# Kernel optimization log

Hardware: AMD Instinct MI355X
Metric: run time of the kernel (lower is better)

## Reference

```python
import jax, jax.numpy as jnp
import numpy as np

N = 100000
E = 1600000
IN_C = 128
OUT_C = 128


def setup_inputs() -> dict:
    key = jax.random.key(0)
    k1, k2, k3, k4, k5, k6 = jax.random.split(key, 6)
    x = jax.random.normal(k1, (N, IN_C), dtype=jnp.float32)
    edge_row = jax.random.randint(k2, (E,), 0, N, dtype=jnp.int32)  # dst nodes
    edge_col = jax.random.randint(k3, (E,), 0, N, dtype=jnp.int32)  # src nodes
    scale = 1.0 / np.sqrt(IN_C)
    W_l = jax.random.normal(k4, (IN_C, OUT_C), dtype=jnp.float32) * scale
    b_l = jax.random.normal(k5, (OUT_C,), dtype=jnp.float32) * 0.01
    W_r = jax.random.normal(k6, (IN_C, OUT_C), dtype=jnp.float32) * scale
    return {"x": x, "edge_row": edge_row, "edge_col": edge_col,
            "W_l": W_l, "b_l": b_l, "W_r": W_r}


def reference(x, edge_row, edge_col, W_l, b_l, W_r):
    # SAGEConv with mean aggregation over adj_t (edge_row=dst, edge_col=src)
    msgs = x[edge_col]                                   # [E, IN_C] gather
    summed = jax.ops.segment_sum(msgs, edge_row, num_segments=N)  # [N, IN_C]
    deg = jax.ops.segment_sum(jnp.ones((E,), dtype=x.dtype), edge_row,
                              num_segments=N)            # [N]
    agg = summed / jnp.maximum(deg, 1.0)[:, None]        # mean aggregation
    out = agg @ W_l + b_l + x @ W_r                      # lin_l(agg) + lin_r(x_dst)
    return jax.nn.relu(out)
```

## Files before the change

kernel.cpp:

```cpp
#include <hip/hip_runtime.h>

#define N_NODES 100000
#define E_EDGES 1600000
#define C 128
#define BSHIFT 10
#define NBKT 98
#define CAP 18432

typedef __attribute__((ext_vector_type(8))) short short8;
typedef __attribute__((ext_vector_type(4))) float f32x4;

__device__ __forceinline__ unsigned short f2bf(float f) {
  unsigned int b = __float_as_uint(f);
  return (unsigned short)((b + 0x7fffu + ((b >> 16) & 1u)) >> 16);
}
__device__ __forceinline__ float bflo(unsigned int v) {
  return __uint_as_float(v << 16);
}
__device__ __forceinline__ float bfhi(unsigned int v) {
  return __uint_as_float(v & 0xffff0000u);
}

__global__ __launch_bounds__(256) void cvt_kernel(const float* __restrict__ x,
                                                  ushort* __restrict__ xh) {
  int t = blockIdx.x * 256 + threadIdx.x;
  float4 a = ((const float4*)x)[2 * t];
  float4 b = ((const float4*)x)[2 * t + 1];
  ushort u[8] = {f2bf(a.x), f2bf(a.y), f2bf(a.z), f2bf(a.w),
                 f2bf(b.x), f2bf(b.y), f2bf(b.z), f2bf(b.w)};
  ((uint4*)xh)[t] = *(const uint4*)u;
}

__global__ __launch_bounds__(256) void pack_kernel(const float* __restrict__ W_l,
                                                   const float* __restrict__ W_r,
                                                   ushort* __restrict__ Bp) {
  int t = blockIdx.x * 256 + threadIdx.x;
  int Cb = t >> 9, kb = (t >> 6) & 7, lane = t & 63;
  int n = Cb * 16 + (lane & 15);
  int k0 = kb * 32 + (lane >> 4) * 8;
  ushort u[8];
#pragma unroll
  for (int j = 0; j < 8; ++j) {
    int k = k0 + j;
    float w = (k < C) ? W_l[k * C + n] : W_r[(k - C) * C + n];
    u[j] = f2bf(w);
  }
  ((uint4*)Bp)[t] = *(const uint4*)u;
}

__global__ __launch_bounds__(512) void passA_kernel(
    const int* __restrict__ erow, const int* __restrict__ ecol,
    int* __restrict__ bcnt, int* __restrict__ pairs) {
  __shared__ int cnt[NBKT], pos[NBKT], loff[NBKT], total;
  __shared__ int lbuf[2048];
  __shared__ int gaddr[2048];
  int tid = threadIdx.x;
  int idx = blockIdx.x * 512 + tid;
  for (int b = tid; b < NBKT; b += 512) cnt[b] = 0;
  __syncthreads();

  bool ok = (idx < E_EDGES / 4);
  int4 r, c;
  int bk[4], rk[4];
  if (ok) {
    r = ((const int4*)erow)[idx];
    c = ((const int4*)ecol)[idx];
    bk[0] = r.x >> BSHIFT; rk[0] = atomicAdd(&cnt[bk[0]], 1);
    bk[1] = r.y >> BSHIFT; rk[1] = atomicAdd(&cnt[bk[1]], 1);
    bk[2] = r.z >> BSHIFT; rk[2] = atomicAdd(&cnt[bk[2]], 1);
    bk[3] = r.w >> BSHIFT; rk[3] = atomicAdd(&cnt[bk[3]], 1);
  }
  __syncthreads();

  if (tid < NBKT) pos[tid] = atomicAdd(&bcnt[tid], cnt[tid]);
  if (tid == 0) {
    int run = 0;
    for (int b = 0; b < NBKT; ++b) { loff[b] = run; run += cnt[b]; }
    total = run;
  }
  __syncthreads();

  if (ok) {
    int src[4] = {c.x, c.y, c.z, c.w};
    int dst[4] = {r.x, r.y, r.z, r.w};
#pragma unroll
    for (int i = 0; i < 4; ++i) {
      int s = loff[bk[i]] + rk[i];
      lbuf[s] = (src[i] << BSHIFT) | (dst[i] & (  (1<<BSHIFT) - 1));
      int g = pos[bk[i]] + rk[i];
      gaddr[s] = (g < CAP) ? bk[i] * CAP + g : -1;
    }
  }
  __syncthreads();

  int tot = total;
  for (int i = tid; i < tot; i += 512) {
    int g = gaddr[i];
    if (g >= 0) pairs[g] = lbuf[i];
  }
}

__global__ __launch_bounds__(128) void bscan_kernel(const int* __restrict__ bcnt,
                                                    int* __restrict__ bbase) {
  __shared__ int l[128];
  int t = threadIdx.x;
  int v = (t < NBKT) ? min(bcnt[t], CAP) : 0;
  l[t] = v;
  __syncthreads();
  for (int d = 1; d < 128; d <<= 1) {
    int u = (t >= d) ? l[t - d] : 0;
    __syncthreads();
    l[t] += u;
    __syncthreads();
  }
  if (t < NBKT) bbase[t] = l[t] - v;
}

__global__ __launch_bounds__(1024) void passB_kernel(
    const int* __restrict__ pairs, const int* __restrict__ bcnt,
    const int* __restrict__ bbase, int* __restrict__ off,
    int* __restrict__ ssrc) {
  __shared__ int l[1024];
  __shared__ int cur[1024];
  int b = blockIdx.x, t = threadIdx.x;
  int nbase = b << BSHIFT;
  int nn = min(1024, N_NODES - nbase);
  int cnt = min(bcnt[b], CAP);
  int gbase = bbase[b];
  const int* bp = pairs + b * CAP;

  l[t] = 0;
  __syncthreads();
  for (int e = t; e < cnt; e += 1024) atomicAdd(&l[bp[e] & 1023], 1);
  __syncthreads();
  int own = l[t];
  for (int d = 1; d < 1024; d <<= 1) {
    int u = (t >= d) ? l[t - d] : 0;
    __syncthreads();
    l[t] += u;
    __syncthreads();
  }
  int excl = l[t] - own;
  if (t < nn) { off[nbase + t] = gbase + excl; cur[t] = excl; }
  if (b == NBKT - 1 && t == 1023) off[N_NODES] = gbase + l[1023];
  __syncthreads();
  for (int e = t; e < cnt; e += 1024) {
    int p = bp[e];
    int pos = atomicAdd(&cur[p & 1023], 1);
    ssrc[gbase + pos] = p >> BSHIFT;
  }
}

__global__ __launch_bounds__(256) void fused_kernel(
    const ushort* __restrict__ xh, const int* __restrict__ off,
    const int* __restrict__ ssrc, const ushort* __restrict__ Bp,
    const float* __restrict__ b_l, float* __restrict__ out) {
  __shared__ ushort lA[32][264];
  int tid = threadIdx.x;
  int lane = tid & 63;
  int wave = tid >> 6;
  long base = (long)blockIdx.x * 32;

  for (int i = tid; i < 32 * 16; i += 256) {
    int r = i >> 4, q = i & 15;
    uint4 v = ((const uint4*)(xh + (base + r) * C))[q];
    *(uint4*)&lA[r][128 + q * 8] = v;
  }

  int l4 = lane & 15;
  int q = lane >> 4;

  for (int j = 0; j < 8; ++j) {
    int n = wave * 8 + j;
    long row = base + n;
    int e0 = off[row];
    int e1 = off[row + 1];
    float s[8];
#pragma unroll
    for (int i = 0; i < 8; ++i) s[i] = 0.0f;

    int e = e0 + q;
    for (; e + 4 < e1; e += 8) {
      int sa = ssrc[e];
      int sb = ssrc[e + 4];
      uint4 va = ((const uint4*)(xh + (long)sa * C))[l4];
      uint4 vb = ((const uint4*)(xh + (long)sb * C))[l4];
      s[0] += bflo(va.x) + bflo(vb.x); s[1] += bfhi(va.x) + bfhi(vb.x);
      s[2] += bflo(va.y) + bflo(vb.y); s[3] += bfhi(va.y) + bfhi(vb.y);
      s[4] += bflo(va.z) + bflo(vb.z); s[5] += bfhi(va.z) + bfhi(vb.z);
      s[6] += bflo(va.w) + bflo(vb.w); s[7] += bfhi(va.w) + bfhi(vb.w);
    }
    if (e < e1) {
      int sa = ssrc[e];
      uint4 va = ((const uint4*)(xh + (long)sa * C))[l4];
      s[0] += bflo(va.x); s[1] += bfhi(va.x);
      s[2] += bflo(va.y); s[3] += bfhi(va.y);
      s[4] += bflo(va.z); s[5] += bfhi(va.z);
      s[6] += bflo(va.w); s[7] += bfhi(va.w);
    }
#pragma unroll
    for (int i = 0; i < 8; ++i) {
      s[i] += __shfl_xor(s[i], 16);
      s[i] += __shfl_xor(s[i], 32);
    }
    float inv = 1.0f / fmaxf((float)(e1 - e0), 1.0f);
    if (q == 0) {
      ushort u[8];
#pragma unroll
      for (int i = 0; i < 8; ++i) u[i] = f2bf(s[i] * inv);
      *(uint4*)&lA[n][l4 * 8] = *(const uint4*)u;
    }
  }
  __syncthreads();

  f32x4 acc0 = {0, 0, 0, 0}, acc1 = {0, 0, 0, 0};
  f32x4 acc2 = {0, 0, 0, 0}, acc3 = {0, 0, 0, 0};
  int m = lane & 15, quad = lane >> 4;
  const ushort* bp0 = Bp + (((2 * wave + 0) * 8) * 64 + lane) * 8;
  const ushort* bp1 = Bp + (((2 * wave + 1) * 8) * 64 + lane) * 8;
#pragma unroll
  for (int kb = 0; kb < 8; ++kb) {
    short8 a0 = *(const short8*)&lA[m][kb * 32 + quad * 8];
    short8 a1 = *(const short8*)&lA[16 + m][kb * 32 + quad * 8];
    short8 b0 = *(const short8*)(bp0 + kb * 64 * 8);
    short8 b1 = *(const short8*)(bp1 + kb * 64 * 8);
    acc0 = __builtin_amdgcn_mfma_f32_16x16x32_bf16(a0, b0, acc0, 0, 0, 0);
    acc1 = __builtin_amdgcn_mfma_f32_16x16x32_bf16(a0, b1, acc1, 0, 0, 0);
    acc2 = __builtin_amdgcn_mfma_f32_16x16x32_bf16(a1, b0, acc2, 0, 0, 0);
    acc3 = __builtin_amdgcn_mfma_f32_16x16x32_bf16(a1, b1, acc3, 0, 0, 0);
  }

  int col0 = (2 * wave + 0) * 16 + m;
  int col1 = col0 + 16;
  float bl0 = b_l[col0], bl1 = b_l[col1];
#pragma unroll
  for (int r = 0; r < 4; ++r) {
    long row0 = base + quad * 4 + r;
    long row1 = row0 + 16;
    out[row0 * C + col0] = fmaxf(acc0[r] + bl0, 0.0f);
    out[row0 * C + col1] = fmaxf(acc1[r] + bl1, 0.0f);
    out[row1 * C + col0] = fmaxf(acc2[r] + bl0, 0.0f);
    out[row1 * C + col1] = fmaxf(acc3[r] + bl1, 0.0f);
  }
}

extern "C" void kernel_launch(void* const* d_in, const int* in_sizes, int n_in,
                              void* d_out, int out_size, void* d_ws, size_t ws_size,
                              hipStream_t stream) {
  const float* x   = (const float*)d_in[0];
  const int* erow  = (const int*)d_in[1];
  const int* ecol  = (const int*)d_in[2];
  const float* W_l = (const float*)d_in[3];
  const float* b_l = (const float*)d_in[4];
  const float* W_r = (const float*)d_in[5];
  float* out = (float*)d_out;

  char* p = (char*)d_ws;
  ushort* xh  = (ushort*)p;  p += (size_t)N_NODES * C * 2;
  ushort* Bp  = (ushort*)p;  p += 2 * C * C * 2;
  int* off    = (int*)p;     p += (size_t)(N_NODES + 4) * 4;
  int* pairs  = (int*)p;     p += (size_t)NBKT * CAP * 4;
  int* ssrc   = (int*)p;     p += (size_t)E_EDGES * 4;
  int* bcnt   = (int*)p;     p += 128 * 4;
  int* bbase  = (int*)p;

  hipMemsetAsync(bcnt, 0, NBKT * sizeof(int), stream);
  cvt_kernel<<<N_NODES * C / 8 / 256, 256, 0, stream>>>(x, xh);
  pack_kernel<<<(8 * 8 * 64) / 256, 256, 0, stream>>>(W_l, W_r, Bp);
  passA_kernel<<<(E_EDGES / 4 + 511) / 512, 512, 0, stream>>>(erow, ecol, bcnt,
                                                              pairs);
  bscan_kernel<<<1, 128, 0, stream>>>(bcnt, bbase);
  passB_kernel<<<NBKT, 1024, 0, stream>>>(pairs, bcnt, bbase, off, ssrc);
  fused_kernel<<<N_NODES / 32, 256, 0, stream>>>(xh, off, ssrc, Bp, b_l, out);
}
```

Before: 234.8 us.

## Merge preprocessing kernels, fold bucket scan into passB, unroll gather by four

Combines the bf16 conversion, weight packing and edge bucketing into one launch with block-range dispatch, and moves the tiny bucket prefix scan into each passB block, which removes three kernel launches and their serialization gaps. The gather loop in the fused kernel is also unrolled to four neighbor loads per iteration to raise memory-level parallelism. The costs are redundant per-block scans in passB, higher register pressure in the fused kernel, and a merged kernel that mixes heterogeneous block work and shared-memory footprints.

```diff
diff --git a/kernel.cpp b/kernel.cpp
--- a/kernel.cpp
+++ b/kernel.cpp
@@ -7,6 +7,10 @@
 #define NBKT 98
 #define CAP 18432
 
+#define PA_BLOCKS 782
+#define PACK_BLOCKS 8
+#define CVT_BLOCKS 3125
+
 typedef __attribute__((ext_vector_type(8))) short short8;
 typedef __attribute__((ext_vector_type(4))) float f32x4;
 
@@ -21,117 +25,116 @@
   return __uint_as_float(v & 0xffff0000u);
 }
 
-__global__ __launch_bounds__(256) void cvt_kernel(const float* __restrict__ x,
-                                                  ushort* __restrict__ xh) {
-  int t = blockIdx.x * 256 + threadIdx.x;
-  float4 a = ((const float4*)x)[2 * t];
-  float4 b = ((const float4*)x)[2 * t + 1];
-  ushort u[8] = {f2bf(a.x), f2bf(a.y), f2bf(a.z), f2bf(a.w),
-                 f2bf(b.x), f2bf(b.y), f2bf(b.z), f2bf(b.w)};
-  ((uint4*)xh)[t] = *(const uint4*)u;
-}
-
-__global__ __launch_bounds__(256) void pack_kernel(const float* __restrict__ W_l,
-                                                   const float* __restrict__ W_r,
-                                                   ushort* __restrict__ Bp) {
-  int t = blockIdx.x * 256 + threadIdx.x;
-  int Cb = t >> 9, kb = (t >> 6) & 7, lane = t & 63;
-  int n = Cb * 16 + (lane & 15);
-  int k0 = kb * 32 + (lane >> 4) * 8;
-  ushort u[8];
-#pragma unroll
-  for (int j = 0; j < 8; ++j) {
-    int k = k0 + j;
-    float w = (k < C) ? W_l[k * C + n] : W_r[(k - C) * C + n];
-    u[j] = f2bf(w);
-  }
-  ((uint4*)Bp)[t] = *(const uint4*)u;
-}
-
-__global__ __launch_bounds__(512) void passA_kernel(
-    const int* __restrict__ erow, const int* __restrict__ ecol,
-    int* __restrict__ bcnt, int* __restrict__ pairs) {
+__global__ __launch_bounds__(512) void mega_kernel(
+    const float* __restrict__ x, const int* __restrict__ erow,
+    const int* __restrict__ ecol, const float* __restrict__ W_l,
+    const float* __restrict__ W_r, ushort* __restrict__ xh,
+    ushort* __restrict__ Bp, int* __restrict__ bcnt, int* __restrict__ pairs) {
   __shared__ int cnt[NBKT], pos[NBKT], loff[NBKT], total;
   __shared__ int lbuf[2048];
   __shared__ int gaddr[2048];
+  int bid = blockIdx.x;
   int tid = threadIdx.x;
-  int idx = blockIdx.x * 512 + tid;
-  for (int b = tid; b < NBKT; b += 512) cnt[b] = 0;
-  __syncthreads();
-
-  bool ok = (idx < E_EDGES / 4);
-  int4 r, c;
-  int bk[4], rk[4];
-  if (ok) {
-    r = ((const int4*)erow)[idx];
-    c = ((const int4*)ecol)[idx];
-    bk[0] = r.x >> BSHIFT; rk[0] = atomicAdd(&cnt[bk[0]], 1);
-    bk[1] = r.y >> BSHIFT; rk[1] = atomicAdd(&cnt[bk[1]], 1);
-    bk[2] = r.z >> BSHIFT; rk[2] = atomicAdd(&cnt[bk[2]], 1);
-    bk[3] = r.w >> BSHIFT; rk[3] = atomicAdd(&cnt[bk[3]], 1);
-  }
-  __syncthreads();
-
-  if (tid < NBKT) pos[tid] = atomicAdd(&bcnt[tid], cnt[tid]);
-  if (tid == 0) {
-    int run = 0;
-    for (int b = 0; b < NBKT; ++b) { loff[b] = run; run += cnt[b]; }
-    total = run;
-  }
-  __syncthreads();
-
-  if (ok) {
-    int src[4] = {c.x, c.y, c.z, c.w};
-    int dst[4] = {r.x, r.y, r.z, r.w};
-#pragma unroll
-    for (int i = 0; i < 4; ++i) {
-      int s = loff[bk[i]] + rk[i];
-      lbuf[s] = (src[i] << BSHIFT) | (dst[i] & (  (1<<BSHIFT) - 1));
-      int g = pos[bk[i]] + rk[i];
-      gaddr[s] = (g < CAP) ? bk[i] * CAP + g : -1;
-    }
-  }
-  __syncthreads();
-
-  int tot = total;
-  for (int i = tid; i < tot; i += 512) {
-    int g = gaddr[i];
-    if (g >= 0) pairs[g] = lbuf[i];
-  }
-}
-
-__global__ __launch_bounds__(128) void bscan_kernel(const int* __restrict__ bcnt,
-                                                    int* __restrict__ bbase) {
-  __shared__ int l[128];
-  int t = threadIdx.x;
-  int v = (t < NBKT) ? min(bcnt[t], CAP) : 0;
-  l[t] = v;
-  __syncthreads();
-  for (int d = 1; d < 128; d <<= 1) {
-    int u = (t >= d) ? l[t - d] : 0;
-    __syncthreads();
-    l[t] += u;
-    __syncthreads();
-  }
-  if (t < NBKT) bbase[t] = l[t] - v;
+
+  if (bid < PA_BLOCKS) {
+    for (int b = tid; b < NBKT; b += 512) cnt[b] = 0;
+    __syncthreads();
+
+    int idx = bid * 512 + tid;
+    bool ok = (idx < E_EDGES / 4);
+    int4 r, c;
+    int bk[4], rk[4];
+    if (ok) {
+      r = ((const int4*)erow)[idx];
+      c = ((const int4*)ecol)[idx];
+      bk[0] = r.x >> BSHIFT; rk[0] = atomicAdd(&cnt[bk[0]], 1);
+      bk[1] = r.y >> BSHIFT; rk[1] = atomicAdd(&cnt[bk[1]], 1);
+      bk[2] = r.z >> BSHIFT; rk[2] = atomicAdd(&cnt[bk[2]], 1);
+      bk[3] = r.w >> BSHIFT; rk[3] = atomicAdd(&cnt[bk[3]], 1);
+    }
+    __syncthreads();
+
+    if (tid < NBKT) pos[tid] = atomicAdd(&bcnt[tid], cnt[tid]);
+    if (tid == 0) {
+      int run = 0;
+      for (int b = 0; b < NBKT; ++b) { loff[b] = run; run += cnt[b]; }
+      total = run;
+    }
+    __syncthreads();
+
+    if (ok) {
+      int src[4] = {c.x, c.y, c.z, c.w};
+      int dst[4] = {r.x, r.y, r.z, r.w};
+#pragma unroll
+      for (int i = 0; i < 4; ++i) {
+        int s = loff[bk[i]] + rk[i];
+        lbuf[s] = (src[i] << BSHIFT) | (dst[i] & ((1 << BSHIFT) - 1));
+        int g = pos[bk[i]] + rk[i];
+        gaddr[s] = (g < CAP) ? bk[i] * CAP + g : -1;
+      }
+    }
+    __syncthreads();
+
+    int tot = total;
+    for (int i = tid; i < tot; i += 512) {
+      int g = gaddr[i];
+      if (g >= 0) pairs[g] = lbuf[i];
+    }
+  } else if (bid < PA_BLOCKS + PACK_BLOCKS) {
+    int t = (bid - PA_BLOCKS) * 512 + tid;
+    int Cb = t >> 9, kb = (t >> 6) & 7, lane = t & 63;
+    int n = Cb * 16 + (lane & 15);
+    int k0 = kb * 32 + (lane >> 4) * 8;
+    ushort u[8];
+#pragma unroll
+    for (int j = 0; j < 8; ++j) {
+      int k = k0 + j;
+      float w = (k < C) ? W_l[k * C + n] : W_r[(k - C) * C + n];
+      u[j] = f2bf(w);
+    }
+    ((uint4*)Bp)[t] = *(const uint4*)u;
+  } else {
+    int t = (bid - PA_BLOCKS - PACK_BLOCKS) * 512 + tid;
+    float4 a = ((const float4*)x)[2 * t];
+    float4 b = ((const float4*)x)[2 * t + 1];
+    ushort u[8] = {f2bf(a.x), f2bf(a.y), f2bf(a.z), f2bf(a.w),
+                   f2bf(b.x), f2bf(b.y), f2bf(b.z), f2bf(b.w)};
+    ((uint4*)xh)[t] = *(const uint4*)u;
+  }
 }
 
 __global__ __launch_bounds__(1024) void passB_kernel(
     const int* __restrict__ pairs, const int* __restrict__ bcnt,
-    const int* __restrict__ bbase, int* __restrict__ off,
-    int* __restrict__ ssrc) {
+    int* __restrict__ off, int* __restrict__ ssrc) {
   __shared__ int l[1024];
   __shared__ int cur[1024];
+  __shared__ int s_gbase;
   int b = blockIdx.x, t = threadIdx.x;
+
+  int v = 0;
+  if (t < 128) {
+    v = (t < NBKT) ? min(bcnt[t], CAP) : 0;
+    l[t] = v;
+  }
+  __syncthreads();
+  for (int d = 1; d < 128; d <<= 1) {
+    int u = (t >= d && t < 128) ? l[t - d] : 0;
+    __syncthreads();
+    if (t < 128) l[t] += u;
+    __syncthreads();
+  }
+  if (t == b) s_gbase = l[t] - v;
+  __syncthreads();
+
   int nbase = b << BSHIFT;
   int nn = min(1024, N_NODES - nbase);
-  int cnt = min(bcnt[b], CAP);
-  int gbase = bbase[b];
+  int cntb = min(bcnt[b], CAP);
+  int gbase = s_gbase;
   const int* bp = pairs + b * CAP;
 
   l[t] = 0;
   __syncthreads();
-  for (int e = t; e < cnt; e += 1024) atomicAdd(&l[bp[e] & 1023], 1);
+  for (int e = t; e < cntb; e += 1024) atomicAdd(&l[bp[e] & 1023], 1);
   __syncthreads();
   int own = l[t];
   for (int d = 1; d < 1024; d <<= 1) {
@@ -144,10 +147,10 @@
   if (t < nn) { off[nbase + t] = gbase + excl; cur[t] = excl; }
   if (b == NBKT - 1 && t == 1023) off[N_NODES] = gbase + l[1023];
   __syncthreads();
-  for (int e = t; e < cnt; e += 1024) {
+  for (int e = t; e < cntb; e += 1024) {
     int p = bp[e];
-    int pos = atomicAdd(&cur[p & 1023], 1);
-    ssrc[gbase + pos] = p >> BSHIFT;
+    int posn = atomicAdd(&cur[p & 1023], 1);
+    ssrc[gbase + posn] = p >> BSHIFT;
   }
 }
 
@@ -180,9 +183,23 @@
     for (int i = 0; i < 8; ++i) s[i] = 0.0f;
 
     int e = e0 + q;
+    for (; e + 12 < e1; e += 16) {
+      int sa = ssrc[e], sb = ssrc[e + 4], sc = ssrc[e + 8], sd = ssrc[e + 12];
+      uint4 va = ((const uint4*)(xh + (long)sa * C))[l4];
+      uint4 vb = ((const uint4*)(xh + (long)sb * C))[l4];
+      uint4 vc = ((const uint4*)(xh + (long)sc * C))[l4];
+      uint4 vd = ((const uint4*)(xh + (long)sd * C))[l4];
+      s[0] += (bflo(va.x) + bflo(vb.x)) + (bflo(vc.x) + bflo(vd.x));
+      s[1] += (bfhi(va.x) + bfhi(vb.x)) + (bfhi(vc.x) + bfhi(vd.x));
+      s[2] += (bflo(va.y) + bflo(vb.y)) + (bflo(vc.y) + bflo(vd.y));
+      s[3] += (bfhi(va.y) + bfhi(vb.y)) + (bfhi(vc.y) + bfhi(vd.y));
+      s[4] += (bflo(va.z) + bflo(vb.z)) + (bflo(vc.z) + bflo(vd.z));
+      s[5] += (bfhi(va.z) + bfhi(vb.z)) + (bfhi(vc.z) + bfhi(vd.z));
+      s[6] += (bflo(va.w) + bflo(vb.w)) + (bflo(vc.w) + bflo(vd.w));
+      s[7] += (bfhi(va.w) + bfhi(vb.w)) + (bfhi(vc.w) + bfhi(vd.w));
+    }
     for (; e + 4 < e1; e += 8) {
-      int sa = ssrc[e];
-      int sb = ssrc[e + 4];
+      int sa = ssrc[e], sb = ssrc[e + 4];
       uint4 va = ((const uint4*)(xh + (long)sa * C))[l4];
       uint4 vb = ((const uint4*)(xh + (long)sb * C))[l4];
       s[0] += bflo(va.x) + bflo(vb.x); s[1] += bfhi(va.x) + bfhi(vb.x);
@@ -261,15 +278,11 @@
   int* off    = (int*)p;     p += (size_t)(N_NODES + 4) * 4;
   int* pairs  = (int*)p;     p += (size_t)NBKT * CAP * 4;
   int* ssrc   = (int*)p;     p += (size_t)E_EDGES * 4;
-  int* bcnt   = (int*)p;     p += 128 * 4;
-  int* bbase  = (int*)p;
+  int* bcnt   = (int*)p;
 
   hipMemsetAsync(bcnt, 0, NBKT * sizeof(int), stream);
-  cvt_kernel<<<N_NODES * C / 8 / 256, 256, 0, stream>>>(x, xh);
-  pack_kernel<<<(8 * 8 * 64) / 256, 256, 0, stream>>>(W_l, W_r, Bp);
-  passA_kernel<<<(E_EDGES / 4 + 511) / 512, 512, 0, stream>>>(erow, ecol, bcnt,
-                                                              pairs);
-  bscan_kernel<<<1, 128, 0, stream>>>(bcnt, bbase);
-  passB_kernel<<<NBKT, 1024, 0, stream>>>(pairs, bcnt, bbase, off, ssrc);
+  mega_kernel<<<PA_BLOCKS + PACK_BLOCKS + CVT_BLOCKS, 512, 0, stream>>>(
+      x, erow, ecol, W_l, W_r, xh, Bp, bcnt, pairs);
+  passB_kernel<<<NBKT, 1024, 0, stream>>>(pairs, bcnt, off, ssrc);
   fused_kernel<<<N_NODES / 32, 256, 0, stream>>>(xh, off, ssrc, Bp, b_l, out);
 }
```

New measurement: 238.3 us. Within noise of the previous version (+1.5%).
